# Performance work log

Hardware: AMD Instinct MI355X
Metric: run time of the kernel (lower is better)

Reference implementation:

```python
import jax, jax.numpy as jnp
import numpy as np
from jax.ops import segment_sum

N_NODES = 50000


def gcn_conv(x, W, b, src, dst, n_nodes):
    """Standard PyG GCNConv: self-loops + symmetric deg^-1/2 normalization."""
    h = x @ W  # [N, H]
    loop = jnp.arange(n_nodes, dtype=src.dtype)
    s = jnp.concatenate([src, loop])
    d = jnp.concatenate([dst, loop])
    deg = segment_sum(jnp.ones_like(d, dtype=h.dtype), d, num_segments=n_nodes)
    dinv = jnp.where(deg > 0, jax.lax.rsqrt(deg), 0.0)
    norm = dinv[s] * dinv[d]  # [E+N]
    msg = h[s] * norm[:, None]  # gather + scale
    out = segment_sum(msg, d, num_segments=n_nodes)  # scatter-add
    return out + b


def setup_inputs() -> dict:
    key = jax.random.key(0)
    ks = jax.random.split(key, 12)
    node_in, hidden = 256, 128
    n_edges = 1_600_000
    x = jax.random.normal(ks[0], (N_NODES, node_in), dtype=jnp.float32)
    edge_index = jax.random.randint(ks[1], (2, n_edges), 0, N_NODES, dtype=jnp.int64)

    def glorot(k, fan_in, fan_out):
        lim = np.sqrt(6.0 / (fan_in + fan_out)).astype(np.float32)
        return jax.random.uniform(k, (fan_in, fan_out), jnp.float32, -lim, lim)

    W1 = glorot(ks[2], node_in, hidden)
    b1 = jnp.zeros((hidden,), jnp.float32)
    W2 = glorot(ks[3], hidden, hidden)
    b2 = jnp.zeros((hidden,), jnp.float32)
    W3 = glorot(ks[4], 2 * hidden, hidden)
    b3 = jnp.zeros((hidden,), jnp.float32)
    W4 = glorot(ks[5], hidden, 1)
    b4 = jnp.zeros((1,), jnp.float32)
    return {"x": x, "edge_index": edge_index, "W1": W1, "b1": b1,
            "W2": W2, "b2": b2, "W3": W3, "b3": b3, "W4": W4, "b4": b4}


def reference(x, edge_index, W1, b1, W2, b2, W3, b3, W4, b4):
    src, dst = edge_index[0], edge_index[1]
    h = gcn_conv(x, W1, b1, src, dst, N_NODES)
    h = jax.nn.relu(h)  # dropout is identity in eval mode
    h = gcn_conv(h, W2, b2, src, dst, N_NODES)
    # gather node pairs per edge, concat, MLP edge classifier
    ef = jnp.concatenate([h[src], h[dst]], axis=1)  # [E, 2H]
    z = jax.nn.relu(ef @ W3 + b3)
    scores = jax.nn.sigmoid(z @ W4 + b4)
    return scores.squeeze(-1)
```

## Files before the change

kernel.cpp:

```cpp
#include <hip/hip_runtime.h>
#include <math.h>

typedef unsigned short ushort_t;
typedef __attribute__((ext_vector_type(8))) short bf16x8;
typedef __attribute__((ext_vector_type(8))) unsigned short us8;
typedef __attribute__((ext_vector_type(4))) float f32x4;

__device__ __forceinline__ float bf2f(unsigned short u) {
    union { unsigned int i; float f; } x; x.i = ((unsigned int)u) << 16; return x.f;
}
__device__ __forceinline__ unsigned short f2bf(float f) {
    union { float f; unsigned int i; } x; x.f = f;
    unsigned int lsb = (x.i >> 16) & 1u;
    return (unsigned short)((x.i + 0x7fffu + lsb) >> 16);
}


__global__ __launch_bounds__(1024) void detect_i64(const int* __restrict__ ei,
                                                   int nwords, int* __restrict__ flag) {
    __shared__ int s_any;
    if (threadIdx.x == 0) s_any = 0;
    __syncthreads();
    int any = 0;
    for (int i = threadIdx.x; 2 * i + 1 < nwords; i += 1024)
        if (ei[2 * i + 1] != 0) any = 1;
    if (any) s_any = 1;
    __syncthreads();
    if (threadIdx.x == 0) flag[0] = (s_any == 0) ? 1 : 0;
}

__global__ __launch_bounds__(256) void normalize_idx(const int* __restrict__ ei, int E,
                                                     const int* __restrict__ flag,
                                                     int* __restrict__ s_out,
                                                     int* __restrict__ d_out) {
    int e = blockIdx.x * 256 + threadIdx.x;
    if (e >= E) return;
    if (flag[0]) {
        s_out[e] = ei[2 * e];
        d_out[e] = ei[2 * (E + e)];
    } else {
        s_out[e] = ei[e];
        d_out[e] = ei[E + e];
    }
}


__global__ __launch_bounds__(256) void zero_i32(int* __restrict__ p, int n) {
    int i = blockIdx.x * 256 + threadIdx.x;
    if (i < n) p[i] = 0;
}

__global__ __launch_bounds__(256) void count_deg_part(const int* __restrict__ dst,
                                                      int* __restrict__ deg,
                                                      int E, int RB) {
    int xcd = blockIdx.x & 7;
    int e = (blockIdx.x >> 3) * 256 + threadIdx.x;
    if (e >= E) return;
    int d = dst[e];
    if ((unsigned)(d - xcd * RB) < (unsigned)RB) atomicAdd(&deg[d], 1);
}

__global__ __launch_bounds__(1024) void scan_kernel(const int* __restrict__ deg,
                                                    int* __restrict__ offs,
                                                    int* __restrict__ cursor,
                                                    float* __restrict__ dinv, int n) {
    __shared__ int wsum[16];
    __shared__ int s_carry;
    int tid = threadIdx.x, lane = tid & 63, wid = tid >> 6;
    if (tid == 0) s_carry = 0;
    __syncthreads();
    for (int base = 0; base < n; base += 1024) {
        int i = base + tid;
        int v = (i < n) ? deg[i] : 0;
        int x = v;
        #pragma unroll
        for (int d = 1; d < 64; d <<= 1) {
            int y = __shfl_up(x, d, 64);
            if (lane >= d) x += y;
        }
        if (lane == 63) wsum[wid] = x;
        __syncthreads();
        int carry = s_carry;
        __syncthreads();
        if (tid == 0) {
            int run = 0;
            #pragma unroll
            for (int w = 0; w < 16; ++w) { int t = wsum[w]; wsum[w] = run; run += t; }
            s_carry = carry + run;
        }
        __syncthreads();
        if (i < n) {
            int excl = carry + wsum[wid] + (x - v);
            offs[i] = excl;
            cursor[i] = excl;
            dinv[i] = rsqrtf((float)(v + 1));
        }
        __syncthreads();
    }
    if (tid == 0) offs[n] = s_carry;
}

__global__ __launch_bounds__(256) void fill_csr_part(const int* __restrict__ src,
                                                     const int* __restrict__ dst,
                                                     int* __restrict__ cursor,
                                                     int2* __restrict__ csr_se,
                                                     int E, int RB) {
    int xcd = blockIdx.x & 7;
    int e = (blockIdx.x >> 3) * 256 + threadIdx.x;
    if (e >= E) return;
    int d = dst[e];
    if ((unsigned)(d - xcd * RB) < (unsigned)RB) {
        int pos = atomicAdd(&cursor[d], 1);
        csr_se[pos] = make_int2(src[e], e);
    }
}


__global__ __launch_bounds__(256) void conv_weights(const float* __restrict__ W1,
                                                    const float* __restrict__ W2,
                                                    const float* __restrict__ W3,
                                                    ushort_t* __restrict__ Wt1,
                                                    ushort_t* __restrict__ Wt2,
                                                    ushort_t* __restrict__ Wt3a,
                                                    ushort_t* __restrict__ Wt3b) {
    int t = blockIdx.x * 256 + threadIdx.x;
    if (t < 32768) {
        int k = t >> 7, n = t & 127;
        Wt1[n * 256 + k] = f2bf(W1[t]);
    } else if (t < 49152) {
        int u = t - 32768; int k = u >> 7, n = u & 127;
        Wt2[n * 128 + k] = f2bf(W2[u]);
    } else if (t < 65536) {
        int u = t - 49152; int k = u >> 7, n = u & 127;
        Wt3a[n * 128 + k] = f2bf(W3[u]);
    } else if (t < 81920) {
        int u = t - 65536; int k = u >> 7, n = u & 127;
        Wt3b[n * 128 + k] = f2bf(W3[128 * 128 + u]);
    }
}


#define ASTR 40
#define BSTR 136

__global__ __launch_bounds__(256) void gemm_mfma(const float* __restrict__ A,
                                                 const ushort_t* __restrict__ Wt,
                                                 void* __restrict__ outv,
                                                 const float* __restrict__ dinv,
                                                 const float* __restrict__ bias,
                                                 int M, int K, int out_bf16) {
    __shared__ __attribute__((aligned(16))) ushort_t Bt[128 * BSTR];
    __shared__ __attribute__((aligned(16))) ushort_t As[64 * ASTR];
    int tid = threadIdx.x;
    int wave = tid >> 6, lane = tid & 63;
    int l15 = lane & 15, lg = lane >> 4;
    int block_m = blockIdx.x * 64;
    f32x4 acc[8];
    #pragma unroll
    for (int i = 0; i < 8; ++i) acc[i] = (f32x4){0.f, 0.f, 0.f, 0.f};

    for (int kh = 0; kh < K; kh += 128) {
        #pragma unroll
        for (int i = 0; i < 16; ++i) {
            int u = i * 256 + tid;
            int col = u >> 5;
            int kq = (u & 31) * 4;
            ushort4 w = *(const ushort4*)(&Wt[(size_t)col * K + kh + kq]);
            *(ushort4*)(&Bt[col * BSTR + kq]) = w;
        }
        for (int k0 = kh; k0 < kh + 128; k0 += 32) {
            #pragma unroll
            for (int rep = 0; rep < 2; ++rep) {
                int unit = rep * 256 + tid;
                int r = unit >> 3;
                int kc = (unit & 7) * 4;
                int gr = block_m + r;
                int grc = gr < M ? gr : M - 1;
                float4 v = *(const float4*)(&A[(size_t)grc * K + k0 + kc]);
                if (gr >= M) v = make_float4(0.f, 0.f, 0.f, 0.f);
                ushort4 p;
                p.x = f2bf(v.x); p.y = f2bf(v.y); p.z = f2bf(v.z); p.w = f2bf(v.w);
                *(ushort4*)(&As[r * ASTR + kc]) = p;
            }
            __syncthreads();
            bf16x8 af = *(const bf16x8*)(&As[(wave * 16 + l15) * ASTR + lg * 8]);
            #pragma unroll
            for (int nf = 0; nf < 8; ++nf) {
                bf16x8 bf = *(const bf16x8*)(&Bt[(nf * 16 + l15) * BSTR +
                                                 (k0 - kh) + lg * 8]);
                acc[nf] = __builtin_amdgcn_mfma_f32_16x16x32_bf16(af, bf, acc[nf],
                                                                  0, 0, 0);
            }
            __syncthreads();
        }
    }
    int orow = block_m + wave * 16 + lg * 4;
    #pragma unroll
    for (int nf = 0; nf < 8; ++nf) {
        int col = nf * 16 + l15;
        float bb = bias ? bias[col] : 0.f;
        #pragma unroll
        for (int j = 0; j < 4; ++j) {
            int m = orow + j;
            if (m < M) {
                float s = dinv ? dinv[m] : 1.f;
                float o = acc[nf][j] * s + bb;
                if (out_bf16)
                    ((ushort_t*)outv)[(size_t)m * 128 + col] = f2bf(o);
                else
                    ((float*)outv)[(size_t)m * 128 + col] = o;
            }
        }
    }
}


__global__ __launch_bounds__(256) void pull_agg(const ushort_t* __restrict__ g,
                                                const int2* __restrict__ csr_se,
                                                const int* __restrict__ offs,
                                                const float* __restrict__ dinv,
                                                const float* __restrict__ bias,
                                                float* __restrict__ out,
                                                int n_nodes, int do_relu) {
    int tid = threadIdx.x;
    int wid = tid >> 6, lane = tid & 63;
    int q = lane >> 4, c = lane & 15;
    int node = blockIdx.x * 4 + wid;
    if (node >= n_nodes) return;
    int beg = offs[node], end = offs[node + 1];
    float acc[8] = {};
    int i = beg;
    for (; i + 8 <= end; i += 8) {
        int s1 = csr_se[i + q].x;
        int s2 = csr_se[i + 4 + q].x;
        us8 r1 = *(const us8*)(g + (size_t)s1 * 128 + c * 8);
        us8 r2 = *(const us8*)(g + (size_t)s2 * 128 + c * 8);
        acc[0] += bf2f(r1[0]); acc[1] += bf2f(r1[1]);
        acc[2] += bf2f(r1[2]); acc[3] += bf2f(r1[3]);
        acc[4] += bf2f(r1[4]); acc[5] += bf2f(r1[5]);
        acc[6] += bf2f(r1[6]); acc[7] += bf2f(r1[7]);
        acc[0] += bf2f(r2[0]); acc[1] += bf2f(r2[1]);
        acc[2] += bf2f(r2[2]); acc[3] += bf2f(r2[3]);
        acc[4] += bf2f(r2[4]); acc[5] += bf2f(r2[5]);
        acc[6] += bf2f(r2[6]); acc[7] += bf2f(r2[7]);
    }
    for (; i < end; i += 4) {
        int j = i + q;
        int sidx = (j < end) ? csr_se[j].x : n_nodes;
        us8 r = *(const us8*)(g + (size_t)sidx * 128 + c * 8);
        acc[0] += bf2f(r[0]); acc[1] += bf2f(r[1]);
        acc[2] += bf2f(r[2]); acc[3] += bf2f(r[3]);
        acc[4] += bf2f(r[4]); acc[5] += bf2f(r[5]);
        acc[6] += bf2f(r[6]); acc[7] += bf2f(r[7]);
    }
    #pragma unroll
    for (int k = 0; k < 8; ++k) {
        acc[k] += __shfl_xor(acc[k], 16, 64);
        acc[k] += __shfl_xor(acc[k], 32, 64);
    }
    us8 sr = *(const us8*)(g + (size_t)node * 128 + c * 8);
    float s = dinv[node];
    float4 ba = *(const float4*)(&bias[c * 8]);
    float4 bb = *(const float4*)(&bias[c * 8 + 4]);
    float o[8];
    o[0] = (acc[0] + bf2f(sr[0])) * s + ba.x;
    o[1] = (acc[1] + bf2f(sr[1])) * s + ba.y;
    o[2] = (acc[2] + bf2f(sr[2])) * s + ba.z;
    o[3] = (acc[3] + bf2f(sr[3])) * s + ba.w;
    o[4] = (acc[4] + bf2f(sr[4])) * s + bb.x;
    o[5] = (acc[5] + bf2f(sr[5])) * s + bb.y;
    o[6] = (acc[6] + bf2f(sr[6])) * s + bb.z;
    o[7] = (acc[7] + bf2f(sr[7])) * s + bb.w;
    if (do_relu) {
        #pragma unroll
        for (int k = 0; k < 8; ++k) o[k] = fmaxf(o[k], 0.f);
    }
    if (q == 0) {
        float* op = &out[(size_t)node * 128 + c * 8];
        *(float4*)op = make_float4(o[0], o[1], o[2], o[3]);
        *(float4*)(op + 4) = make_float4(o[4], o[5], o[6], o[7]);
    }
}


__device__ __forceinline__ float edot8(const us8& uu, const float* vr,
                                       const float4& wa, const float4& wb) {
    float ps;
    ps  = fmaxf(bf2f(uu[0]) + vr[0], 0.f) * wa.x;
    ps += fmaxf(bf2f(uu[1]) + vr[1], 0.f) * wa.y;
    ps += fmaxf(bf2f(uu[2]) + vr[2], 0.f) * wa.z;
    ps += fmaxf(bf2f(uu[3]) + vr[3], 0.f) * wa.w;
    ps += fmaxf(bf2f(uu[4]) + vr[4], 0.f) * wb.x;
    ps += fmaxf(bf2f(uu[5]) + vr[5], 0.f) * wb.y;
    ps += fmaxf(bf2f(uu[6]) + vr[6], 0.f) * wb.z;
    ps += fmaxf(bf2f(uu[7]) + vr[7], 0.f) * wb.w;
    ps += __shfl_xor(ps, 8, 64);
    ps += __shfl_xor(ps, 4, 64);
    ps += __shfl_xor(ps, 2, 64);
    ps += __shfl_xor(ps, 1, 64);
    return ps;
}

__global__ __launch_bounds__(256) void edge_score_seg(const ushort_t* __restrict__ u,
                                                      const ushort_t* __restrict__ v,
                                                      const int2* __restrict__ csr_se,
                                                      const int* __restrict__ offs,
                                                      const float* __restrict__ W4,
                                                      const float* __restrict__ b4,
                                                      float* __restrict__ out,
                                                      int n_nodes) {
    int tid = threadIdx.x;
    int grp = tid >> 4, c = tid & 15;
    int node = blockIdx.x * 16 + grp;
    if (node >= n_nodes) return;
    int beg = offs[node], end = offs[node + 1];
    if (beg == end) return;
    us8 vv = *(const us8*)(v + (size_t)node * 128 + c * 8);
    float vr[8];
    #pragma unroll
    for (int k = 0; k < 8; ++k) vr[k] = bf2f(vv[k]);
    float4 wa = *(const float4*)(&W4[c * 8]);
    float4 wb = *(const float4*)(&W4[c * 8 + 4]);
    float b4v = b4[0];
    int p = beg;
    for (; p + 4 <= end; p += 4) {
        int2 se0 = csr_se[p];
        int2 se1 = csr_se[p + 1];
        int2 se2 = csr_se[p + 2];
        int2 se3 = csr_se[p + 3];
        us8 u0 = *(const us8*)(u + (size_t)se0.x * 128 + c * 8);
        us8 u1 = *(const us8*)(u + (size_t)se1.x * 128 + c * 8);
        us8 u2 = *(const us8*)(u + (size_t)se2.x * 128 + c * 8);
        us8 u3 = *(const us8*)(u + (size_t)se3.x * 128 + c * 8);
        float p0 = edot8(u0, vr, wa, wb);
        float p1 = edot8(u1, vr, wa, wb);
        float p2 = edot8(u2, vr, wa, wb);
        float p3 = edot8(u3, vr, wa, wb);
        if (c == 0) {
            out[se0.y] = 1.f / (1.f + expf(-(p0 + b4v)));
            out[se1.y] = 1.f / (1.f + expf(-(p1 + b4v)));
            out[se2.y] = 1.f / (1.f + expf(-(p2 + b4v)));
            out[se3.y] = 1.f / (1.f + expf(-(p3 + b4v)));
        }
    }
    for (; p < end; ++p) {
        int2 se = csr_se[p];
        us8 uu = *(const us8*)(u + (size_t)se.x * 128 + c * 8);
        float ps = edot8(uu, vr, wa, wb);
        if (c == 0)
            out[se.y] = 1.f / (1.f + expf(-(ps + b4v)));
    }
}


extern "C" void kernel_launch(void* const* d_in, const int* in_sizes, int n_in,
                              void* d_out, int out_size, void* d_ws, size_t ws_size,
                              hipStream_t stream) {
    const float* x  = (const float*)d_in[0];
    const int*   ei = (const int*)d_in[1];
    const float* W1 = (const float*)d_in[2];
    const float* b1 = (const float*)d_in[3];
    const float* W2 = (const float*)d_in[4];
    const float* b2 = (const float*)d_in[5];
    const float* W3 = (const float*)d_in[6];
    const float* b3 = (const float*)d_in[7];
    const float* W4 = (const float*)d_in[8];
    const float* b4 = (const float*)d_in[9];

    int N = in_sizes[0] / 256;
    int E = in_sizes[1] / 2;

    char* ws = (char*)d_ws;
    size_t off = 0;
    auto alloc = [&](size_t bytes) -> void* {
        void* p = ws + off;
        off += (bytes + 255) & ~(size_t)255;
        return p;
    };
    int*      flag    = (int*)     alloc(256);
    int*      srcn    = (int*)     alloc((size_t)E * 4);
    int*      dstn    = (int*)     alloc((size_t)E * 4);
    int*      deg     = (int*)     alloc((size_t)N * 4);
    int*      offs    = (int*)     alloc((size_t)(N + 1) * 4);
    int*      cursor  = (int*)     alloc((size_t)N * 4);
    float*    dinv    = (float*)   alloc((size_t)N * 4);
    int2*     csr_se  = (int2*)    alloc((size_t)E * 8);
    ushort_t* gbuf    = (ushort_t*)alloc((size_t)(N + 1) * 128 * 2);
    ushort_t* ubuf    = (ushort_t*)alloc((size_t)N * 128 * 2);
    ushort_t* vbuf    = (ushort_t*)alloc((size_t)N * 128 * 2);
    float*    hbuf    = (float*)   alloc((size_t)N * 128 * 4);
    ushort_t* Wt1     = (ushort_t*)alloc(128 * 256 * 2);
    ushort_t* Wt2     = (ushort_t*)alloc(128 * 128 * 2);
    ushort_t* Wt3a    = (ushort_t*)alloc(128 * 128 * 2);
    ushort_t* Wt3b    = (ushort_t*)alloc(128 * 128 * 2);
    (void)ws_size; (void)n_in; (void)out_size;

    float* outp = (float*)d_out;
    int gE = (E + 255) / 256;
    int gN4 = (N + 3) / 4;
    int RB = (N + 7) / 8;

    int nwords = (2 * E < 4096) ? 2 * E : 4096;
    detect_i64<<<1, 1024, 0, stream>>>(ei, nwords, flag);
    normalize_idx<<<gE, 256, 0, stream>>>(ei, E, flag, srcn, dstn);
    conv_weights<<<320, 256, 0, stream>>>(W1, W2, W3, Wt1, Wt2, Wt3a, Wt3b);

    zero_i32<<<(N + 255) / 256, 256, 0, stream>>>(deg, N);
    zero_i32<<<1, 256, 0, stream>>>((int*)(gbuf + (size_t)N * 128), 64);
    count_deg_part<<<gE * 8, 256, 0, stream>>>(dstn, deg, E, RB);
    scan_kernel<<<1, 1024, 0, stream>>>(deg, offs, cursor, dinv, N);
    fill_csr_part<<<gE * 8, 256, 0, stream>>>(srcn, dstn, cursor, csr_se, E, RB);

    int gM = (N + 63) / 64;
    gemm_mfma<<<gM, 256, 0, stream>>>(x, Wt1, gbuf, dinv, nullptr, N, 256, 1);
    pull_agg<<<gN4, 256, 0, stream>>>(gbuf, csr_se, offs, dinv, b1, hbuf, N, 1);
    gemm_mfma<<<gM, 256, 0, stream>>>(hbuf, Wt2, gbuf, dinv, nullptr, N, 128, 1);
    pull_agg<<<gN4, 256, 0, stream>>>(gbuf, csr_se, offs, dinv, b2, hbuf, N, 0);
    gemm_mfma<<<gM, 256, 0, stream>>>(hbuf, Wt3a, ubuf, nullptr, nullptr, N, 128, 1);
    gemm_mfma<<<gM, 256, 0, stream>>>(hbuf, Wt3b, vbuf, nullptr, b3, N, 128, 1);
    edge_score_seg<<<(N + 15) / 16, 256, 0, stream>>>(ubuf, vbuf, csr_se, offs,
                                                      W4, b4, outp, N);
}
```

Baseline: 582.4 us.

## Store hidden activations in bf16 and use register-resident weight GEMM for K=128

The aggregation kernel now writes its hidden output as bf16 instead of fp32, halving the activation buffer and the reads done by the following GEMMs. A new gemm_regB kernel keeps the full 128x128 bf16 weight matrix in registers per wave and runs a persistent grid-stride loop over 16-row tiles, loading A directly from global memory with no LDS staging or barriers. The fp32 A path of gemm_mfma is kept only for the first layer. The trade-off is heavy register use (32 bf16x8 fragments per lane), which may limit occupancy, plus an extra bf16 rounding of the intermediate activations.

Result: no change. 580.0 us (-0.4%).

```diff
diff --git a/kernel.cpp b/kernel.cpp
--- a/kernel.cpp
+++ b/kernel.cpp
@@ -145,10 +145,10 @@
 
 __global__ __launch_bounds__(256) void gemm_mfma(const float* __restrict__ A,
                                                  const ushort_t* __restrict__ Wt,
-                                                 void* __restrict__ outv,
+                                                 ushort_t* __restrict__ outp,
                                                  const float* __restrict__ dinv,
                                                  const float* __restrict__ bias,
-                                                 int M, int K, int out_bf16) {
+                                                 int M, int K) {
     __shared__ __attribute__((aligned(16))) ushort_t Bt[128 * BSTR];
     __shared__ __attribute__((aligned(16))) ushort_t As[64 * ASTR];
     int tid = threadIdx.x;
@@ -204,11 +204,63 @@
             int m = orow + j;
             if (m < M) {
                 float s = dinv ? dinv[m] : 1.f;
-                float o = acc[nf][j] * s + bb;
-                if (out_bf16)
-                    ((ushort_t*)outv)[(size_t)m * 128 + col] = f2bf(o);
-                else
-                    ((float*)outv)[(size_t)m * 128 + col] = o;
+                outp[(size_t)m * 128 + col] = f2bf(acc[nf][j] * s + bb);
+            }
+        }
+    }
+}
+
+
+__global__ __launch_bounds__(256) void gemm_regB(const ushort_t* __restrict__ A,
+                                                 const ushort_t* __restrict__ Wt,
+                                                 ushort_t* __restrict__ outp,
+                                                 const float* __restrict__ dinv,
+                                                 const float* __restrict__ bias,
+                                                 int M) {
+    int tid = threadIdx.x;
+    int wave = tid >> 6, lane = tid & 63;
+    int l15 = lane & 15, lg = lane >> 4;
+    bf16x8 Bf[8][4];
+    #pragma unroll
+    for (int nf = 0; nf < 8; ++nf)
+        #pragma unroll
+        for (int ks = 0; ks < 4; ++ks)
+            Bf[nf][ks] = *(const bf16x8*)(&Wt[(size_t)(nf * 16 + l15) * 128 +
+                                              ks * 32 + lg * 8]);
+    float bv[8];
+    #pragma unroll
+    for (int nf = 0; nf < 8; ++nf)
+        bv[nf] = bias ? bias[nf * 16 + l15] : 0.f;
+
+    int nt = (M + 15) >> 4;
+    for (int tile = blockIdx.x * 4 + wave; tile < nt; tile += gridDim.x * 4) {
+        int r = tile * 16 + l15;
+        const ushort_t* Ar = A + (size_t)(r < M ? r : M - 1) * 128;
+        bf16x8 af0 = *(const bf16x8*)(Ar + 0 * 32 + lg * 8);
+        bf16x8 af1 = *(const bf16x8*)(Ar + 1 * 32 + lg * 8);
+        bf16x8 af2 = *(const bf16x8*)(Ar + 2 * 32 + lg * 8);
+        bf16x8 af3 = *(const bf16x8*)(Ar + 3 * 32 + lg * 8);
+        f32x4 acc[8];
+        #pragma unroll
+        for (int i = 0; i < 8; ++i) acc[i] = (f32x4){0.f, 0.f, 0.f, 0.f};
+        #pragma unroll
+        for (int nf = 0; nf < 8; ++nf) {
+            acc[nf] = __builtin_amdgcn_mfma_f32_16x16x32_bf16(af0, Bf[nf][0], acc[nf], 0, 0, 0);
+            acc[nf] = __builtin_amdgcn_mfma_f32_16x16x32_bf16(af1, Bf[nf][1], acc[nf], 0, 0, 0);
+            acc[nf] = __builtin_amdgcn_mfma_f32_16x16x32_bf16(af2, Bf[nf][2], acc[nf], 0, 0, 0);
+            acc[nf] = __builtin_amdgcn_mfma_f32_16x16x32_bf16(af3, Bf[nf][3], acc[nf], 0, 0, 0);
+        }
+        int orow = tile * 16 + lg * 4;
+        #pragma unroll
+        for (int nf = 0; nf < 8; ++nf) {
+            int col = nf * 16 + l15;
+            #pragma unroll
+            for (int j = 0; j < 4; ++j) {
+                int m = orow + j;
+                if (m < M) {
+                    float s = dinv ? dinv[m] : 1.f;
+                    outp[(size_t)m * 128 + col] = f2bf(acc[nf][j] * s + bv[nf]);
+                }
             }
         }
     }
@@ -220,7 +272,7 @@
                                                 const int* __restrict__ offs,
                                                 const float* __restrict__ dinv,
                                                 const float* __restrict__ bias,
-                                                float* __restrict__ out,
+                                                ushort_t* __restrict__ out,
                                                 int n_nodes, int do_relu) {
     int tid = threadIdx.x;
     int wid = tid >> 6, lane = tid & 63;
@@ -276,9 +328,10 @@
         for (int k = 0; k < 8; ++k) o[k] = fmaxf(o[k], 0.f);
     }
     if (q == 0) {
-        float* op = &out[(size_t)node * 128 + c * 8];
-        *(float4*)op = make_float4(o[0], o[1], o[2], o[3]);
-        *(float4*)(op + 4) = make_float4(o[4], o[5], o[6], o[7]);
+        us8 w;
+        #pragma unroll
+        for (int k = 0; k < 8; ++k) w[k] = f2bf(o[k]);
+        *(us8*)(out + (size_t)node * 128 + c * 8) = w;
     }
 }
 
@@ -388,7 +441,7 @@
     ushort_t* gbuf    = (ushort_t*)alloc((size_t)(N + 1) * 128 * 2);
     ushort_t* ubuf    = (ushort_t*)alloc((size_t)N * 128 * 2);
     ushort_t* vbuf    = (ushort_t*)alloc((size_t)N * 128 * 2);
-    float*    hbuf    = (float*)   alloc((size_t)N * 128 * 4);
+    ushort_t* hbuf    = (ushort_t*)alloc((size_t)N * 128 * 2);
     ushort_t* Wt1     = (ushort_t*)alloc(128 * 256 * 2);
     ushort_t* Wt2     = (ushort_t*)alloc(128 * 128 * 2);
     ushort_t* Wt3a    = (ushort_t*)alloc(128 * 128 * 2);
@@ -412,12 +465,12 @@
     fill_csr_part<<<gE * 8, 256, 0, stream>>>(srcn, dstn, cursor, csr_se, E, RB);
 
     int gM = (N + 63) / 64;
-    gemm_mfma<<<gM, 256, 0, stream>>>(x, Wt1, gbuf, dinv, nullptr, N, 256, 1);
+    gemm_mfma<<<gM, 256, 0, stream>>>(x, Wt1, gbuf, dinv, nullptr, N, 256);
     pull_agg<<<gN4, 256, 0, stream>>>(gbuf, csr_se, offs, dinv, b1, hbuf, N, 1);
-    gemm_mfma<<<gM, 256, 0, stream>>>(hbuf, Wt2, gbuf, dinv, nullptr, N, 128, 1);
+    gemm_regB<<<512, 256, 0, stream>>>(hbuf, Wt2, gbuf, dinv, nullptr, N);
     pull_agg<<<gN4, 256, 0, stream>>>(gbuf, csr_se, offs, dinv, b2, hbuf, N, 0);
-    gemm_mfma<<<gM, 256, 0, stream>>>(hbuf, Wt3a, ubuf, nullptr, nullptr, N, 128, 1);
-    gemm_mfma<<<gM, 256, 0, stream>>>(hbuf, Wt3b, vbuf, nullptr, b3, N, 128, 1);
+    gemm_regB<<<512, 256, 0, stream>>>(hbuf, Wt3a, ubuf, nullptr, nullptr, N);
+    gemm_regB<<<512, 256, 0, stream>>>(hbuf, Wt3b, vbuf, nullptr, b3, N);
     edge_score_seg<<<(N + 15) / 16, 256, 0, stream>>>(ubuf, vbuf, csr_se, offs,
                                                       W4, b4, outp, N);
 }
```
